# Performance work log

Hardware: AMD Instinct MI355X
Metric: run time of the kernel (lower is better)

The kernel has to match this reference:

```python
import jax, jax.numpy as jnp
import numpy as np

D_MODEL = 768
N_HEADS = 12
D_HEAD = 64
BATCH = 4
SEQ = 2048
INIT_RANGE = 0.02
IGNORE = -1e5


def setup_inputs() -> dict:
    key = jax.random.key(0)
    ks = jax.random.split(key, 5)
    x = jax.random.normal(ks[0], (BATCH, SEQ, D_MODEL), dtype=jnp.float32)
    W_Q = jax.random.normal(ks[1], (N_HEADS, D_MODEL, D_HEAD), dtype=jnp.float32) * INIT_RANGE
    W_K = jax.random.normal(ks[2], (N_HEADS, D_MODEL, D_HEAD), dtype=jnp.float32) * INIT_RANGE
    W_V = jax.random.normal(ks[3], (N_HEADS, D_MODEL, D_HEAD), dtype=jnp.float32) * INIT_RANGE
    W_O = jax.random.normal(ks[4], (N_HEADS, D_HEAD, D_MODEL), dtype=jnp.float32) * INIT_RANGE
    b_Q = jnp.zeros((N_HEADS, D_HEAD), dtype=jnp.float32)
    b_K = jnp.zeros((N_HEADS, D_HEAD), dtype=jnp.float32)
    b_V = jnp.zeros((N_HEADS, D_HEAD), dtype=jnp.float32)
    b_O = jnp.zeros((D_MODEL,), dtype=jnp.float32)
    return {"normalized_resid_pre": x, "W_Q": W_Q, "W_K": W_K, "W_V": W_V,
            "W_O": W_O, "b_Q": b_Q, "b_K": b_K, "b_V": b_V, "b_O": b_O}


def reference(normalized_resid_pre, W_Q, W_K, W_V, W_O, b_Q, b_K, b_V, b_O):
    x = normalized_resid_pre  # [b, s, d_model]
    q = jnp.einsum('bsm,hmd->bshd', x, W_Q) + b_Q  # [b, s, h, d_head]
    k = jnp.einsum('bsm,hmd->bshd', x, W_K) + b_K
    v = jnp.einsum('bsm,hmd->bshd', x, W_V) + b_V
    scores = jnp.einsum('bqhd,bkhd->bhqk', q, k) / jnp.sqrt(jnp.float32(D_HEAD))
    seq = x.shape[1]
    causal = jnp.tril(jnp.ones((seq, seq), dtype=bool))  # True where allowed
    scores = jnp.where(causal, scores, jnp.float32(IGNORE))
    pattern = jax.nn.softmax(scores, axis=-1)  # [b, h, q, k]
    z = jnp.einsum('bhqk,bkhd->bqhd', pattern, v)
    attn_out = jnp.einsum('bqhd,hdm->bqm', z, W_O) + b_O
    return attn_out
```

## Files before the change

kernel.cpp:

```cpp
#include <hip/hip_runtime.h>
#include <math.h>

#define DEVI __device__ __forceinline__

typedef __bf16 bf16_t;
typedef bf16_t bf16x8 __attribute__((ext_vector_type(8)));
typedef float  f32x4  __attribute__((ext_vector_type(4)));

constexpr int NB   = 4;
constexpr int SEQL = 2048;
constexpr int NH   = 12;
constexpr int DHD  = 64;
constexpr int DMOD = 768;
constexpr int NT   = NB * SEQL;
constexpr int KD   = DMOD;


DEVI unsigned short f2bf(float f) {
  union { float f; unsigned u; } v; v.f = f;
  unsigned r = v.u + 0x7FFFu + ((v.u >> 16) & 1u);
  return (unsigned short)(r >> 16);
}

DEVI unsigned short cvt_bf16(float f) {
  bf16_t b = (bf16_t)f;
  return __builtin_bit_cast(unsigned short, b);
}

DEVI float exp2_raw(float x) {
  float r;
  asm("v_exp_f32 %0, %1" : "=v"(r) : "v"(x));
  return r;
}

DEVI void gload16(const unsigned short* src, unsigned short* dst) {
  auto g = (const __attribute__((address_space(1))) unsigned int*)(unsigned long long)src;
  auto l = (__attribute__((address_space(3))) unsigned int*)(unsigned int)(unsigned long long)(dst);
  __builtin_amdgcn_global_load_lds(g, l, 16, 0, 0);
}

__global__ void __launch_bounds__(256) prep_all(const float* __restrict__ x,
                                                const float* __restrict__ WQ,
                                                const float* __restrict__ WK,
                                                const float* __restrict__ WV,
                                                const float* __restrict__ WO,
                                                unsigned short* __restrict__ xb,
                                                unsigned short* __restrict__ Wt,
                                                unsigned short* __restrict__ Wo_t) {
  __shared__ float T[64][68];
  const int bid = blockIdx.x;
  const int t = threadIdx.x;
  if (bid < 3072) {
    size_t i = ((size_t)bid * 256 + t) * 8;
    float4 a = *(const float4*)(x + i);
    float4 b = *(const float4*)(x + i + 4);
    union { unsigned short u[8]; uint4 v; } pk;
    pk.u[0] = f2bf(a.x); pk.u[1] = f2bf(a.y); pk.u[2] = f2bf(a.z); pk.u[3] = f2bf(a.w);
    pk.u[4] = f2bf(b.x); pk.u[5] = f2bf(b.y); pk.u[6] = f2bf(b.z); pk.u[7] = f2bf(b.w);
    *(uint4*)(xb + i) = pk.v;
    return;
  }
  const int r0 = t >> 4, c4 = (t & 15) * 4;
  if (bid < 3504) {
    const int u = bid - 3072;
    const int mt = u % 12, hw = u / 12;
    const int which = hw / 12, h = hw % 12;
    const float* W = (which == 0) ? WQ : ((which == 1) ? WK : WV);
    const float* src = W + ((size_t)h * 768 + mt * 64) * 64;
#pragma unroll
    for (int rep = 0; rep < 4; ++rep) {
      int m = rep * 16 + r0;
      float4 v = *(const float4*)(src + m * 64 + c4);
      T[m][c4] = v.x; T[m][c4 + 1] = v.y; T[m][c4 + 2] = v.z; T[m][c4 + 3] = v.w;
    }
    __syncthreads();
    unsigned short* dst = Wt + ((size_t)which * 768 + h * 64) * 768 + mt * 64;
#pragma unroll
    for (int rep = 0; rep < 4; ++rep) {
      int d = rep * 16 + r0;
      union { unsigned short u[4]; uint2 v; } o;
#pragma unroll
      for (int j = 0; j < 4; ++j) o.u[j] = f2bf(T[c4 + j][d]);
      *(uint2*)(dst + (size_t)d * 768 + c4) = o.v;
    }
  } else {
    const int u = bid - 3504;
    const int m0 = (u % 12) * 64, hd0 = (u / 12) * 64;
#pragma unroll
    for (int rep = 0; rep < 4; ++rep) {
      int i = rep * 16 + r0;
      float4 v = *(const float4*)(WO + (size_t)(hd0 + i) * 768 + m0 + c4);
      T[i][c4] = v.x; T[i][c4 + 1] = v.y; T[i][c4 + 2] = v.z; T[i][c4 + 3] = v.w;
    }
    __syncthreads();
#pragma unroll
    for (int rep = 0; rep < 4; ++rep) {
      int m = rep * 16 + r0;
      union { unsigned short u[4]; uint2 v; } o;
#pragma unroll
      for (int j = 0; j < 4; ++j) o.u[j] = f2bf(T[c4 + j][m]);
      *(uint2*)(Wo_t + (size_t)(m0 + m) * 768 + hd0 + c4) = o.v;
    }
  }
}

__global__ void __launch_bounds__(256)
gemm_qkv(const unsigned short* __restrict__ A,
         const unsigned short* __restrict__ Bt,
         const float* __restrict__ bq, const float* __restrict__ bk,
         const float* __restrict__ bv,
         unsigned short* __restrict__ qo, unsigned short* __restrict__ ko,
         unsigned short* __restrict__ vo) {
  __shared__ __align__(16) unsigned short ldsA[2 * 8192];
  __shared__ __align__(16) unsigned short ldsB[8192];
  const int bm = blockIdx.x, bn = blockIdx.y;
  const int m0 = bm * 128, n0 = bn * 128;
  const int tid = threadIdx.x, w = tid >> 6, lane = tid & 63;
  const int g = lane >> 4, r16 = lane & 15;
  const int wm = w >> 1, wn = w & 1;

  const int ss = (lane & 7) ^ ((lane >> 3) & 7);
  const unsigned short* asrc = A  + (size_t)(m0 + (lane >> 3)) * KD + ss * 8;
  const unsigned short* bsrc = Bt + (size_t)(n0 + (lane >> 3)) * KD + ss * 8;

  auto stageA = [&](int buf, int kt) {
#pragma unroll
    for (int j = 0; j < 4; ++j) {
      int seg = w * 4 + j;
      gload16(asrc + (size_t)(seg * 8) * KD + kt * 64, ldsA + buf * 8192 + seg * 512);
    }
  };
  auto stageB = [&](int kt) {
#pragma unroll
    for (int j = 0; j < 4; ++j) {
      int seg = w * 4 + j;
      gload16(bsrc + (size_t)(seg * 8) * KD + kt * 64, ldsB + seg * 512);
    }
  };

  const int r7 = r16 & 7;
  const int aoff0 = r16 * 64 + ((g    ) ^ r7) * 8;
  const int aoff1 = r16 * 64 + ((g + 4) ^ r7) * 8;

  f32x4 acc[4][4];
  const f32x4 zero4 = {0.f, 0.f, 0.f, 0.f};
#pragma unroll
  for (int i = 0; i < 4; ++i)
#pragma unroll
    for (int j = 0; j < 4; ++j) acc[i][j] = zero4;

  constexpr int NKT = KD / 64;
  stageA(0, 0);
  stageB(0);
  int buf = 0;
  for (int kt = 0; kt < NKT; ++kt) {
    if (kt + 1 < NKT) {
      stageA(buf ^ 1, kt + 1);
      asm volatile("s_waitcnt vmcnt(4)" ::: "memory");
    } else {
      asm volatile("s_waitcnt vmcnt(0)" ::: "memory");
    }
    __builtin_amdgcn_s_barrier();
    const unsigned short* Ab = ldsA + buf * 8192 + wm * 4096;
    const unsigned short* Bb = ldsB + wn * 4096;
    bf16x8 af[2][4], bfr[2][4];
#pragma unroll
    for (int f = 0; f < 4; ++f) {
      af[0][f]  = *(const bf16x8*)&Ab[aoff0 + f * 1024];
      af[1][f]  = *(const bf16x8*)&Ab[aoff1 + f * 1024];
      bfr[0][f] = *(const bf16x8*)&Bb[aoff0 + f * 1024];
      bfr[1][f] = *(const bf16x8*)&Bb[aoff1 + f * 1024];
    }
#pragma unroll
    for (int kk = 0; kk < 2; ++kk)
#pragma unroll
      for (int fm = 0; fm < 4; ++fm)
#pragma unroll
        for (int fn = 0; fn < 4; ++fn)
          acc[fm][fn] = __builtin_amdgcn_mfma_f32_16x16x32_bf16(af[kk][fm], bfr[kk][fn],
                                                                acc[fm][fn], 0, 0, 0);
    asm volatile("s_waitcnt lgkmcnt(0)" ::: "memory");
    __builtin_amdgcn_s_barrier();
    if (kt + 1 < NKT) stageB(kt + 1);
    buf ^= 1;
  }

#pragma unroll
  for (int fm = 0; fm < 4; ++fm) {
#pragma unroll
    for (int fn = 0; fn < 4; ++fn) {
      const int col = n0 + wn * 64 + fn * 16 + r16;
      const int rbase = m0 + wm * 64 + fm * 16 + g * 4;
      const int which = (col >= 1536) ? 2 : ((col >= 768) ? 1 : 0);
      const int hd = col - which * 768;
      const int h = hd >> 6, d = hd & 63;
      const float bias = (which == 0 ? bq : which == 1 ? bk : bv)[hd];
      if (which == 2) {
        union { unsigned short u[4]; uint2 v; } o;
#pragma unroll
        for (int r = 0; r < 4; ++r) o.u[r] = cvt_bf16(acc[fm][fn][r] + bias);
        const int b = rbase >> 11, s = rbase & (SEQL - 1);
        *(uint2*)(vo + ((size_t)(b * NH + h) * DHD + d) * SEQL + s) = o.v;
      } else {
#pragma unroll
        for (int r = 0; r < 4; ++r) {
          int row = rbase + r;
          int b = row >> 11, s = row & (SEQL - 1);
          float v = acc[fm][fn][r] + bias;
          if (which == 0)
            qo[((size_t)(b * NH + h) * SEQL + s) * DHD + d] = cvt_bf16(v * 0.1803368801111f);
          else
            ko[((size_t)(b * NH + h) * SEQL + s) * DHD + d] = cvt_bf16(v);
        }
      }
    }
  }
}

__global__ void __launch_bounds__(256)
gemm_o(const unsigned short* __restrict__ A,
       const unsigned short* __restrict__ Bt,
       const float* __restrict__ bo, float* __restrict__ fout) {
  __shared__ __align__(16) unsigned short ldsA[2 * 4096];
  __shared__ __align__(16) unsigned short ldsB[8192];
  const int bm = blockIdx.x, bn = blockIdx.y;
  const int m0 = bm * 64, n0 = bn * 128;
  const int tid = threadIdx.x, w = tid >> 6, lane = tid & 63;
  const int g = lane >> 4, r16 = lane & 15;
  const int wm = w >> 1, wn = w & 1;

  const int ss = (lane & 7) ^ ((lane >> 3) & 7);
  const unsigned short* asrc = A  + (size_t)(m0 + (lane >> 3)) * KD + ss * 8;
  const unsigned short* bsrc = Bt + (size_t)(n0 + (lane >> 3)) * KD + ss * 8;

  auto stageA = [&](int buf, int kt) {
#pragma unroll
    for (int j = 0; j < 2; ++j) {
      int seg = w * 2 + j;
      gload16(asrc + (size_t)(seg * 8) * KD + kt * 64, ldsA + buf * 4096 + seg * 512);
    }
  };
  auto stageB = [&](int kt) {
#pragma unroll
    for (int j = 0; j < 4; ++j) {
      int seg = w * 4 + j;
      gload16(bsrc + (size_t)(seg * 8) * KD + kt * 64, ldsB + seg * 512);
    }
  };

  const int r7 = r16 & 7;
  const int aoff0 = r16 * 64 + ((g    ) ^ r7) * 8;
  const int aoff1 = r16 * 64 + ((g + 4) ^ r7) * 8;

  f32x4 acc[2][4];
  const f32x4 zero4 = {0.f, 0.f, 0.f, 0.f};
#pragma unroll
  for (int i = 0; i < 2; ++i)
#pragma unroll
    for (int j = 0; j < 4; ++j) acc[i][j] = zero4;

  constexpr int NKT = KD / 64;
  stageA(0, 0);
  stageB(0);
  int buf = 0;
  for (int kt = 0; kt < NKT; ++kt) {
    if (kt + 1 < NKT) {
      stageA(buf ^ 1, kt + 1);
      asm volatile("s_waitcnt vmcnt(2)" ::: "memory");
    } else {
      asm volatile("s_waitcnt vmcnt(0)" ::: "memory");
    }
    __builtin_amdgcn_s_barrier();
    const unsigned short* Ab = ldsA + buf * 4096 + wm * 2048;
    const unsigned short* Bb = ldsB + wn * 4096;
    bf16x8 af[2][2], bfr[2][4];
#pragma unroll
    for (int f = 0; f < 2; ++f) {
      af[0][f] = *(const bf16x8*)&Ab[aoff0 + f * 1024];
      af[1][f] = *(const bf16x8*)&Ab[aoff1 + f * 1024];
    }
#pragma unroll
    for (int f = 0; f < 4; ++f) {
      bfr[0][f] = *(const bf16x8*)&Bb[aoff0 + f * 1024];
      bfr[1][f] = *(const bf16x8*)&Bb[aoff1 + f * 1024];
    }
#pragma unroll
    for (int kk = 0; kk < 2; ++kk)
#pragma unroll
      for (int fm = 0; fm < 2; ++fm)
#pragma unroll
        for (int fn = 0; fn < 4; ++fn)
          acc[fm][fn] = __builtin_amdgcn_mfma_f32_16x16x32_bf16(af[kk][fm], bfr[kk][fn],
                                                                acc[fm][fn], 0, 0, 0);
    asm volatile("s_waitcnt lgkmcnt(0)" ::: "memory");
    __builtin_amdgcn_s_barrier();
    if (kt + 1 < NKT) stageB(kt + 1);
    buf ^= 1;
  }

#pragma unroll
  for (int fm = 0; fm < 2; ++fm) {
#pragma unroll
    for (int fn = 0; fn < 4; ++fn) {
      const int col = n0 + wn * 64 + fn * 16 + r16;
      const int rbase = m0 + wm * 32 + fm * 16 + g * 4;
      const float bias = bo[col];
#pragma unroll
      for (int r = 0; r < 4; ++r)
        fout[(size_t)(rbase + r) * DMOD + col] = acc[fm][fn][r] + bias;
    }
  }
}

__global__ void __launch_bounds__(256, 3)
attn_fwd(const unsigned short* __restrict__ qb,
         const unsigned short* __restrict__ kb,
         const unsigned short* __restrict__ vt,
         unsigned short* __restrict__ zb) {
  __shared__ __align__(16) unsigned short ldsK[2 * 4096];
  __shared__ __align__(16) unsigned short ldsV[2 * 4096];
  __shared__ __align__(16) unsigned short ldsP[2 * 4096];
  const int id = blockIdx.x;
  const int qp = id / 48, bh = id % 48;
  const int qtA = qp, qtB = 31 - qp;
  const int tid = threadIdx.x, w = tid >> 6, lane = tid & 63;
  const int g = lane >> 4, r16 = lane & 15;
  const int r7 = r16 & 7;

  const int sslot = (lane & 7) ^ (lane >> 3);
  const unsigned short* ksrc = kb + (size_t)bh * SEQL * DHD + (lane >> 3) * 64 + sslot * 8;
  const unsigned short* vsrc = vt + (size_t)bh * SEQL * DHD + (lane >> 3) * 2048 + sslot * 8;

  auto stage = [&](int buf, int kv0) {
#pragma unroll
    for (int j = 0; j < 2; ++j) {
      int seg = w * 2 + j;
      gload16(ksrc + kv0 * 64 + seg * 512, ldsK + buf * 4096 + seg * 512);
      gload16(vsrc + kv0 + seg * 16384,    ldsV + buf * 4096 + seg * 512);
    }
  };

  const int roff0 = r16 * 64 + ((g    ) ^ r7) * 8;
  const int roff1 = r16 * 64 + ((g + 4) ^ r7) * 8;
  char* const pwbA = (char*)ldsP + w * 2048;
  char* const pwbB = (char*)ldsP + 8192 + w * 2048;
  int paddr[4];
#pragma unroll
  for (int fn = 0; fn < 4; ++fn)
    paddr[fn] = r16 * 128 + ((((fn * 2) + (g >> 1)) ^ r7) << 4) + ((g & 1) << 3);
  const int prd0 = r16 * 128 + (((g    ) ^ r7) << 4);
  const int prd1 = r16 * 128 + (((g + 4) ^ r7) << 4);
  const int thr = w * 16 + r16 - g * 4;

  bf16x8 qfA[2], qfB[2];
  {
    const unsigned short* qa = qb + ((size_t)bh * SEQL + qtA * 64 + w * 16 + r16) * DHD + g * 8;
    const unsigned short* qc = qb + ((size_t)bh * SEQL + qtB * 64 + w * 16 + r16) * DHD + g * 8;
    qfA[0] = *(const bf16x8*)qa; qfA[1] = *(const bf16x8*)(qa + 32);
    qfB[0] = *(const bf16x8*)qc; qfB[1] = *(const bf16x8*)(qc + 32);
  }

  const bf16_t one1 = (bf16_t)1.0f;
  const bf16x8 ones = {one1, one1, one1, one1, one1, one1, one1, one1};

  f32x4 zaccA[4], zaccB[4], saccA[4], saccB[4], lsumA, lsumB;
  const f32x4 zero4 = {0.f, 0.f, 0.f, 0.f};
#pragma unroll
  for (int r = 0; r < 4; ++r) { zaccA[r] = zero4; zaccB[r] = zero4; }
  lsumA = zero4; lsumB = zero4;

  auto sm = [&](f32x4* sacc, char* pwb, bool diag) {
    if (diag) {
#pragma unroll
      for (int fn = 0; fn < 4; ++fn)
#pragma unroll
        for (int r = 0; r < 4; ++r)
          if (fn * 16 + r > thr) sacc[fn][r] = -3.0e38f;
    }
#pragma unroll
    for (int fn = 0; fn < 4; ++fn) {
      float p0 = exp2_raw(sacc[fn][0]), p1 = exp2_raw(sacc[fn][1]);
      float p2 = exp2_raw(sacc[fn][2]), p3 = exp2_raw(sacc[fn][3]);
      unsigned w0, w1;
      asm("v_cvt_pk_bf16_f32 %0, %1, %2" : "=v"(w0) : "v"(p0), "v"(p1));
      asm("v_cvt_pk_bf16_f32 %0, %1, %2" : "=v"(w1) : "v"(p2), "v"(p3));
      uint2 pk; pk.x = w0; pk.y = w1;
      *(uint2*)(pwb + paddr[fn]) = pk;
    }
  };

  auto pv2 = [&](bool do2, const unsigned short* Vb) {
    bf16x8 pB0 = *(const bf16x8*)(pwbB + prd0);
    bf16x8 pB1 = *(const bf16x8*)(pwbB + prd1);
    bf16x8 pA0, pA1;
    if (do2) { pA0 = *(const bf16x8*)(pwbA + prd0); pA1 = *(const bf16x8*)(pwbA + prd1); }
#pragma unroll
    for (int fn = 0; fn < 4; ++fn) {
      bf16x8 vf = *(const bf16x8*)&Vb[roff0 + fn * 1024];
      zaccB[fn] = __builtin_amdgcn_mfma_f32_16x16x32_bf16(pB0, vf, zaccB[fn], 0, 0, 0);
      if (do2) zaccA[fn] = __builtin_amdgcn_mfma_f32_16x16x32_bf16(pA0, vf, zaccA[fn], 0, 0, 0);
    }
    lsumB = __builtin_amdgcn_mfma_f32_16x16x32_bf16(pB0, ones, lsumB, 0, 0, 0);
    if (do2) lsumA = __builtin_amdgcn_mfma_f32_16x16x32_bf16(pA0, ones, lsumA, 0, 0, 0);
#pragma unroll
    for (int fn = 0; fn < 4; ++fn) {
      bf16x8 vf = *(const bf16x8*)&Vb[roff1 + fn * 1024];
      zaccB[fn] = __builtin_amdgcn_mfma_f32_16x16x32_bf16(pB1, vf, zaccB[fn], 0, 0, 0);
      if (do2) zaccA[fn] = __builtin_amdgcn_mfma_f32_16x16x32_bf16(pA1, vf, zaccA[fn], 0, 0, 0);
    }
    lsumB = __builtin_amdgcn_mfma_f32_16x16x32_bf16(pB1, ones, lsumB, 0, 0, 0);
    if (do2) lsumA = __builtin_amdgcn_mfma_f32_16x16x32_bf16(pA1, ones, lsumA, 0, 0, 0);
  };

  stage(0, 0);

  for (int kt = 0; kt <= qtB; ++kt) {
    __builtin_amdgcn_s_barrier();
    asm volatile("s_waitcnt vmcnt(0)" ::: "memory");
    const bool doA = (kt <= qtA);
    const unsigned short* Kb = ldsK + (kt & 1) * 4096;
    __builtin_amdgcn_s_setprio(1);
#pragma unroll
    for (int fn = 0; fn < 4; ++fn) {
      bf16x8 kf = *(const bf16x8*)&Kb[roff0 + fn * 1024];
      saccB[fn] = __builtin_amdgcn_mfma_f32_16x16x32_bf16(kf, qfB[0], zero4, 0, 0, 0);
      if (doA) saccA[fn] = __builtin_amdgcn_mfma_f32_16x16x32_bf16(kf, qfA[0], zero4, 0, 0, 0);
    }
#pragma unroll
    for (int fn = 0; fn < 4; ++fn) {
      bf16x8 kf = *(const bf16x8*)&Kb[roff1 + fn * 1024];
      saccB[fn] = __builtin_amdgcn_mfma_f32_16x16x32_bf16(kf, qfB[1], saccB[fn], 0, 0, 0);
      if (doA) saccA[fn] = __builtin_amdgcn_mfma_f32_16x16x32_bf16(kf, qfA[1], saccA[fn], 0, 0, 0);
    }
    if (kt) {
      asm volatile("" ::: "memory");
      pv2(kt - 1 <= qtA, ldsV + ((kt - 1) & 1) * 4096);
    }
    __builtin_amdgcn_s_setprio(0);
    __builtin_amdgcn_s_barrier();
    if (kt < qtB) stage((kt + 1) & 1, (kt + 1) * 64);
    sm(saccB, pwbB, kt == qtB);
    if (doA) sm(saccA, pwbA, kt == qtA);
  }

  asm volatile("" ::: "memory");
  {
    const unsigned short* Vb = ldsV + (qtB & 1) * 4096;
    bf16x8 pB0 = *(const bf16x8*)(pwbB + prd0);
    bf16x8 pB1 = *(const bf16x8*)(pwbB + prd1);
#pragma unroll
    for (int fn = 0; fn < 4; ++fn) {
      bf16x8 vf = *(const bf16x8*)&Vb[roff0 + fn * 1024];
      zaccB[fn] = __builtin_amdgcn_mfma_f32_16x16x32_bf16(pB0, vf, zaccB[fn], 0, 0, 0);
    }
    lsumB = __builtin_amdgcn_mfma_f32_16x16x32_bf16(pB0, ones, lsumB, 0, 0, 0);
#pragma unroll
    for (int fn = 0; fn < 4; ++fn) {
      bf16x8 vf = *(const bf16x8*)&Vb[roff1 + fn * 1024];
      zaccB[fn] = __builtin_amdgcn_mfma_f32_16x16x32_bf16(pB1, vf, zaccB[fn], 0, 0, 0);
    }
    lsumB = __builtin_amdgcn_mfma_f32_16x16x32_bf16(pB1, ones, lsumB, 0, 0, 0);
  }

  const int b = bh / NH, h = bh % NH;
#pragma unroll
  for (int r = 0; r < 4; ++r) {
    float iar = 1.0f / lsumA[r];
    float ibr = 1.0f / lsumB[r];
    int sA = qtA * 64 + w * 16 + g * 4 + r;
    int sB = qtB * 64 + w * 16 + g * 4 + r;
#pragma unroll
    for (int fn = 0; fn < 4; ++fn) {
      int d = fn * 16 + r16;
      zb[((size_t)(b * SEQL + sA)) * DMOD + h * DHD + d] = cvt_bf16(zaccA[fn][r] * iar);
      zb[((size_t)(b * SEQL + sB)) * DMOD + h * DHD + d] = cvt_bf16(zaccB[fn][r] * ibr);
    }
  }
}


extern "C" void kernel_launch(void* const* d_in, const int* in_sizes, int n_in,
                              void* d_out, int out_size, void* d_ws, size_t ws_size,
                              hipStream_t stream) {
  const float* x  = (const float*)d_in[0];
  const float* WQ = (const float*)d_in[1];
  const float* WK = (const float*)d_in[2];
  const float* WV = (const float*)d_in[3];
  const float* WO = (const float*)d_in[4];
  const float* bQ = (const float*)d_in[5];
  const float* bK = (const float*)d_in[6];
  const float* bV = (const float*)d_in[7];
  const float* bO = (const float*)d_in[8];
  float* out = (float*)d_out;

  constexpr size_t NE = (size_t)NT * DMOD;
  unsigned short* w0   = (unsigned short*)d_ws;
  unsigned short* Wqkv = w0;
  unsigned short* Wo   = Wqkv + (size_t)3 * 768 * 768;
  unsigned short* xb   = Wo + (size_t)768 * 768;
  unsigned short* qb   = xb + NE;
  unsigned short* kb   = qb + NE;
  unsigned short* vt   = kb + NE;
  unsigned short* zb   = xb;
  size_t need = (size_t)(vt + NE - w0) * sizeof(unsigned short);
  if (ws_size < need) return;

  prep_all<<<3648, 256, 0, stream>>>(x, WQ, WK, WV, WO, xb, Wqkv, Wo);
  gemm_qkv<<<dim3(64, 18), 256, 0, stream>>>(xb, Wqkv, bQ, bK, bV, qb, kb, vt);
  attn_fwd<<<768, 256, 0, stream>>>(qb, kb, vt, zb);
  gemm_o<<<dim3(128, 6), 256, 0, stream>>>(zb, Wo, bO, out);
}
```

Before: 113.6 us.

## Pair adjacent query tiles per block and restructure KV prefetch pipeline

Each attention block now processes two adjacent causal query tiles instead of a mirrored (qp, 31-qp) pair, and the block order alternates light and heavy pairs. Because both tiles now use nearly every staged K/V tile, fewer tiles are loaded without being fully used. The loop is also restructured: the next K/V tile is prefetched at the top of each iteration under a partial vmcnt wait, and the PV product runs in the same iteration instead of being deferred to the next one, wrapped in a raised s_setprio. The cost is that per-block work is now unequal, so performance depends on how the scheduler spreads blocks across CUs, and PV can no longer overlap with the next QK step.

```diff
diff --git a/kernel.cpp b/kernel.cpp
--- a/kernel.cpp
+++ b/kernel.cpp
@@ -321,8 +321,9 @@
   __shared__ __align__(16) unsigned short ldsV[2 * 4096];
   __shared__ __align__(16) unsigned short ldsP[2 * 4096];
   const int id = blockIdx.x;
-  const int qp = id / 48, bh = id % 48;
-  const int qtA = qp, qtB = 31 - qp;
+  const int kap = id / 48, bh = id % 48;
+  const int k2 = (kap & 1) ? (15 - (kap >> 1)) : (kap >> 1);
+  const int qtA = 2 * k2, qtB = 2 * k2 + 1;
   const int tid = threadIdx.x, w = tid >> 6, lane = tid & 63;
   const int g = lane >> 4, r16 = lane & 15;
   const int r7 = r16 & 7;
@@ -394,6 +395,7 @@
     bf16x8 pB1 = *(const bf16x8*)(pwbB + prd1);
     bf16x8 pA0, pA1;
     if (do2) { pA0 = *(const bf16x8*)(pwbA + prd0); pA1 = *(const bf16x8*)(pwbA + prd1); }
+    __builtin_amdgcn_s_setprio(1);
 #pragma unroll
     for (int fn = 0; fn < 4; ++fn) {
       bf16x8 vf = *(const bf16x8*)&Vb[roff0 + fn * 1024];
@@ -410,15 +412,24 @@
     }
     lsumB = __builtin_amdgcn_mfma_f32_16x16x32_bf16(pB1, ones, lsumB, 0, 0, 0);
     if (do2) lsumA = __builtin_amdgcn_mfma_f32_16x16x32_bf16(pA1, ones, lsumA, 0, 0, 0);
+    __builtin_amdgcn_s_setprio(0);
   };
 
   stage(0, 0);
+  asm volatile("s_waitcnt vmcnt(0)" ::: "memory");
+  __builtin_amdgcn_s_barrier();
 
   for (int kt = 0; kt <= qtB; ++kt) {
-    __builtin_amdgcn_s_barrier();
-    asm volatile("s_waitcnt vmcnt(0)" ::: "memory");
+    if (kt) __builtin_amdgcn_s_barrier();
+    if (kt < qtB) {
+      stage((kt + 1) & 1, (kt + 1) * 64);
+      if (kt) asm volatile("s_waitcnt vmcnt(4)" ::: "memory");
+    } else {
+      asm volatile("s_waitcnt vmcnt(0)" ::: "memory");
+    }
     const bool doA = (kt <= qtA);
     const unsigned short* Kb = ldsK + (kt & 1) * 4096;
+    const unsigned short* Vb = ldsV + (kt & 1) * 4096;
     __builtin_amdgcn_s_setprio(1);
 #pragma unroll
     for (int fn = 0; fn < 4; ++fn) {
@@ -432,34 +443,11 @@
       saccB[fn] = __builtin_amdgcn_mfma_f32_16x16x32_bf16(kf, qfB[1], saccB[fn], 0, 0, 0);
       if (doA) saccA[fn] = __builtin_amdgcn_mfma_f32_16x16x32_bf16(kf, qfA[1], saccA[fn], 0, 0, 0);
     }
-    if (kt) {
-      asm volatile("" ::: "memory");
-      pv2(kt - 1 <= qtA, ldsV + ((kt - 1) & 1) * 4096);
-    }
     __builtin_amdgcn_s_setprio(0);
-    __builtin_amdgcn_s_barrier();
-    if (kt < qtB) stage((kt + 1) & 1, (kt + 1) * 64);
     sm(saccB, pwbB, kt == qtB);
     if (doA) sm(saccA, pwbA, kt == qtA);
-  }
-
-  asm volatile("" ::: "memory");
-  {
-    const unsigned short* Vb = ldsV + (qtB & 1) * 4096;
-    bf16x8 pB0 = *(const bf16x8*)(pwbB + prd0);
-    bf16x8 pB1 = *(const bf16x8*)(pwbB + prd1);
-#pragma unroll
-    for (int fn = 0; fn < 4; ++fn) {
-      bf16x8 vf = *(const bf16x8*)&Vb[roff0 + fn * 1024];
-      zaccB[fn] = __builtin_amdgcn_mfma_f32_16x16x32_bf16(pB0, vf, zaccB[fn], 0, 0, 0);
-    }
-    lsumB = __builtin_amdgcn_mfma_f32_16x16x32_bf16(pB0, ones, lsumB, 0, 0, 0);
-#pragma unroll
-    for (int fn = 0; fn < 4; ++fn) {
-      bf16x8 vf = *(const bf16x8*)&Vb[roff1 + fn * 1024];
-      zaccB[fn] = __builtin_amdgcn_mfma_f32_16x16x32_bf16(pB1, vf, zaccB[fn], 0, 0, 0);
-    }
-    lsumB = __builtin_amdgcn_mfma_f32_16x16x32_bf16(pB1, ones, lsumB, 0, 0, 0);
+    asm volatile("" ::: "memory");
+    pv2(doA, Vb);
   }
 
   const int b = bh / NH, h = bh % NH;
```

Result: slower. 153.1 us (+34.8%).
